# Kernel optimization log

Hardware: AMD Instinct MI355X
Metric: run time of the kernel (lower is better)

The kernel has to match this reference:

```python
import jax, jax.numpy as jnp
import numpy as np

N_NODES = 20000
N_EDGES = 320000
IN_DIM = 512
NUM_CLASSES = 10
DROP_P = 0.2


def _gcn_conv(x, src, dst, W, b, n):
    # PyG GCNConv: linear transform, add self-loops, symmetric deg^-1/2 norm,
    # scatter-add into destination nodes, then bias.
    h = x @ W                                   # [N, out]
    loops = jnp.arange(n)
    s = jnp.concatenate([src, loops])           # source (j)
    d = jnp.concatenate([dst, loops])           # destination (i)
    deg = jax.ops.segment_sum(jnp.ones_like(s, dtype=h.dtype), d, num_segments=n)
    dinv = jax.lax.rsqrt(deg)                   # deg >= 1 thanks to self-loops
    norm = dinv[s] * dinv[d]                    # [E+N]
    msg = h[s] * norm[:, None]                  # gather + per-edge scale
    out = jax.ops.segment_sum(msg, d, num_segments=n)  # scatter-add
    return out + b


def _dropout(x, key, p=DROP_P):
    keep = jax.random.bernoulli(key, 1.0 - p, x.shape)
    return jnp.where(keep, x / (1.0 - p), jnp.zeros((), x.dtype))


def setup_inputs() -> dict:
    key = jax.random.key(0)
    ks = jax.random.split(key, 6)
    x = jax.random.normal(ks[0], (N_NODES, IN_DIM), dtype=jnp.float32)
    edge_index = jax.random.randint(ks[1], (2, N_EDGES), 0, N_NODES, dtype=jnp.int64)
    h1, h2 = IN_DIM // 2, IN_DIM // 4
    W1 = jax.random.normal(ks[2], (IN_DIM, h1), dtype=jnp.float32) / np.sqrt(IN_DIM)
    W2 = jax.random.normal(ks[3], (h1, h2), dtype=jnp.float32) / np.sqrt(h1)
    W3 = jax.random.normal(ks[4], (h2, NUM_CLASSES), dtype=jnp.float32) / np.sqrt(h2)
    b1 = jnp.zeros((h1,), jnp.float32)
    b2 = jnp.zeros((h2,), jnp.float32)
    b3 = jnp.zeros((NUM_CLASSES,), jnp.float32)
    return {"x": x, "edge_index": edge_index, "W1": W1, "b1": b1,
            "W2": W2, "b2": b2, "W3": W3, "b3": b3}


def reference(x, edge_index, W1, b1, W2, b2, W3, b3):
    n = x.shape[0]
    src, dst = edge_index[0], edge_index[1]
    dk1, dk2 = jax.random.split(jax.random.key(1))
    h = _gcn_conv(x, src, dst, W1, b1, n)
    h = _dropout(jax.nn.relu(h), dk1)
    h = _gcn_conv(h, src, dst, W2, b2, n)
    h = _dropout(jax.nn.relu(h), dk2)
    h = _gcn_conv(h, src, dst, W3, b3, n)
    return jax.nn.log_softmax(h, axis=1)
```

## Files before the change

kernel.cpp:

```cpp
#include <hip/hip_runtime.h>
#include <hip/hip_bf16.h>
#include <math.h>

typedef __attribute__((ext_vector_type(8))) short short8;
typedef __attribute__((ext_vector_type(8))) unsigned short ushort8;
typedef __attribute__((ext_vector_type(4))) float f32x4;

__host__ __device__ inline void threefry2x32(unsigned k0, unsigned k1,
                                             unsigned x0, unsigned x1,
                                             unsigned* out0, unsigned* out1) {
  unsigned ks0 = k0, ks1 = k1, ks2 = k0 ^ k1 ^ 0x1BD11BDAu;
  x0 += ks0; x1 += ks1;
#define TF_ROUND(r) { x0 += x1; x1 = (x1 << (r)) | (x1 >> (32 - (r))); x1 ^= x0; }
  TF_ROUND(13) TF_ROUND(15) TF_ROUND(26) TF_ROUND(6)
  x0 += ks1; x1 += ks2 + 1u;
  TF_ROUND(17) TF_ROUND(29) TF_ROUND(16) TF_ROUND(24)
  x0 += ks2; x1 += ks0 + 2u;
  TF_ROUND(13) TF_ROUND(15) TF_ROUND(26) TF_ROUND(6)
  x0 += ks0; x1 += ks1 + 3u;
  TF_ROUND(17) TF_ROUND(29) TF_ROUND(16) TF_ROUND(24)
  x0 += ks1; x1 += ks2 + 4u;
  TF_ROUND(13) TF_ROUND(15) TF_ROUND(26) TF_ROUND(6)
  x0 += ks2; x1 += ks0 + 5u;
#undef TF_ROUND
  *out0 = x0; *out1 = x1;
}

__device__ inline float jax_uniform01(unsigned key0, unsigned key1, unsigned i) {
  unsigned o0, o1;
  threefry2x32(key0, key1, 0u, i, &o0, &o1);
  unsigned bits = o0 ^ o1;
  return __uint_as_float((bits >> 9) | 0x3f800000u) - 1.0f;
}

__device__ inline unsigned short f2bf(float f) {
  unsigned u = __float_as_uint(f);
  u += 0x7fffu + ((u >> 16) & 1u);
  return (unsigned short)(u >> 16);
}

__device__ inline float bf2f(unsigned short b) {
  return __uint_as_float(((unsigned)b) << 16);
}

__global__ void k_zero(int* p, int n) {
  int i = blockIdx.x * blockDim.x + threadIdx.x;
  if (i < n) p[i] = 0;
}

__global__ void k_deg(const int* __restrict__ ei, int E, int* __restrict__ deg) {
  int e = blockIdx.x * blockDim.x + threadIdx.x;
  if (e >= E) return;
  atomicAdd(&deg[ei[E + e]], 1);
}

__global__ __launch_bounds__(256) void k_bsum(const int* __restrict__ deg,
                                              int* __restrict__ bsum, int n) {
  int i = blockIdx.x * 256 + threadIdx.x;
  int v = (i < n) ? deg[i] : 0;
#pragma unroll
  for (int o = 32; o; o >>= 1) v += __shfl_down(v, o);
  __shared__ int ws[4];
  if ((threadIdx.x & 63) == 0) ws[threadIdx.x >> 6] = v;
  __syncthreads();
  if (threadIdx.x == 0) bsum[blockIdx.x] = ws[0] + ws[1] + ws[2] + ws[3];
}

__global__ void k_bscan(int* __restrict__ bsum, int nb) {
  __shared__ int s[128];
  int t = threadIdx.x;
  int v = (t < nb) ? bsum[t] : 0;
  s[t] = v;
  __syncthreads();
  for (int d = 1; d < 128; d <<= 1) {
    int u = (t >= d) ? s[t - d] : 0;
    __syncthreads();
    s[t] += u;
    __syncthreads();
  }
  if (t < nb) bsum[t] = (t == 0) ? 0 : s[t - 1];
}

__global__ __launch_bounds__(256) void k_scatter(const int* __restrict__ deg,
                                                 const int* __restrict__ bsum,
                                                 int* __restrict__ off, int* __restrict__ cur,
                                                 float* __restrict__ dinv, int n) {
  int i = blockIdx.x * 256 + threadIdx.x;
  int d = (i < n) ? deg[i] : 0;
  int lane = threadIdx.x & 63, w = threadIdx.x >> 6;
  int inc = d;
#pragma unroll
  for (int o = 1; o < 64; o <<= 1) {
    int u = __shfl_up(inc, o);
    if (lane >= o) inc += u;
  }
  __shared__ int wsum[4];
  if (lane == 63) wsum[w] = inc;
  __syncthreads();
  int wbase = 0;
  for (int k = 0; k < w; ++k) wbase += wsum[k];
  int excl = inc - d + wbase + bsum[blockIdx.x];
  if (i < n) {
    off[i] = excl;
    cur[i] = excl;
    dinv[i] = 1.0f / sqrtf((float)(d + 1));
    if (i == n - 1) off[n] = excl + d;
  }
}

__global__ void k_fill(const int* __restrict__ ei, int E,
                       int* __restrict__ cur, int* __restrict__ srcs) {
  int e = blockIdx.x * blockDim.x + threadIdx.x;
  if (e >= E) return;
  int s = ei[e];
  int d = ei[E + e];
  int pos = atomicAdd(&cur[d], 1);
  srcs[pos] = s;
}

__global__ void k_cvt_all(const float* __restrict__ W1, unsigned short* __restrict__ W1T,
                          const float* __restrict__ W2, unsigned short* __restrict__ W2T) {
  const int S1 = 512 * 256, S2 = 256 * 128;
  int idx = blockIdx.x * blockDim.x + threadIdx.x;
  if (idx < S1) {
    int k = idx / 256, n = idx % 256;
    W1T[(size_t)n * 512 + k] = f2bf(W1[idx]);
  } else if (idx < S1 + S2) {
    int i2 = idx - S1;
    int k = i2 / 128, n = i2 % 128;
    W2T[(size_t)n * 256 + k] = f2bf(W2[i2]);
  }
}

template <int NF, bool AF32, bool OBF>
__global__ __launch_bounds__(256) void k_gemm_mfma(const void* __restrict__ Ap,
                                                   const unsigned short* __restrict__ BT,
                                                   void* __restrict__ Cp,
                                                   int M, int N, int K) {
  constexpr int BN = 32 * NF;
  __shared__ unsigned short As[64][40];
  __shared__ unsigned short Bs[BN][40];
  const int tid = threadIdx.x;
  const int row0 = blockIdx.y * 64;
  const int col0 = blockIdx.x * BN;
  const int w = tid >> 6, lane = tid & 63;
  const int wm = w >> 1, wn = w & 1;
  const int lr = lane & 15, lk = lane >> 4;

  f32x4 acc[2][NF];
#pragma unroll
  for (int mi = 0; mi < 2; ++mi)
#pragma unroll
    for (int ni = 0; ni < NF; ++ni) acc[mi][ni] = (f32x4)0.0f;

  const int ar = tid >> 2;
  const int aseg = (tid & 3) * 8;

  for (int k0 = 0; k0 < K; k0 += 32) {
    {
      int grow = row0 + ar;
      ushort8 av = (ushort8)0;
      if (grow < M) {
        if (AF32) {
          const float* A = (const float*)Ap;
          const float* p = &A[(size_t)grow * K + k0 + aseg];
          float4 v0 = *(const float4*)p;
          float4 v1 = *(const float4*)(p + 4);
          av[0] = f2bf(v0.x); av[1] = f2bf(v0.y); av[2] = f2bf(v0.z); av[3] = f2bf(v0.w);
          av[4] = f2bf(v1.x); av[5] = f2bf(v1.y); av[6] = f2bf(v1.z); av[7] = f2bf(v1.w);
        } else {
          const unsigned short* A = (const unsigned short*)Ap;
          av = *(const ushort8*)&A[(size_t)grow * K + k0 + aseg];
        }
      }
      *(ushort8*)&As[ar][aseg] = av;
    }
#pragma unroll
    for (int p = 0; p < BN / 64; ++p) {
      int u = tid + p * 256;
      int br = u >> 2;
      int bseg = (u & 3) * 8;
      ushort8 bv = *(const ushort8*)&BT[(size_t)(col0 + br) * K + k0 + bseg];
      *(ushort8*)&Bs[br][bseg] = bv;
    }
    __syncthreads();

    short8 a[2], b[NF];
#pragma unroll
    for (int mi = 0; mi < 2; ++mi)
      a[mi] = *(const short8*)&As[wm * 32 + mi * 16 + lr][lk * 8];
#pragma unroll
    for (int ni = 0; ni < NF; ++ni)
      b[ni] = *(const short8*)&Bs[wn * (BN / 2) + ni * 16 + lr][lk * 8];
#pragma unroll
    for (int mi = 0; mi < 2; ++mi)
#pragma unroll
      for (int ni = 0; ni < NF; ++ni)
        acc[mi][ni] = __builtin_amdgcn_mfma_f32_16x16x32_bf16(a[mi], b[ni], acc[mi][ni], 0, 0, 0);
    __syncthreads();
  }

#pragma unroll
  for (int mi = 0; mi < 2; ++mi) {
    int rbase = row0 + wm * 32 + mi * 16 + lk * 4;
#pragma unroll
    for (int j = 0; j < 4; ++j) {
      int row = rbase + j;
      if (row < M) {
#pragma unroll
        for (int ni = 0; ni < NF; ++ni) {
          int col = col0 + wn * (BN / 2) + ni * 16 + lr;
          if (OBF) {
            ((unsigned short*)Cp)[(size_t)row * N + col] = f2bf(acc[mi][ni][j]);
          } else {
            ((float*)Cp)[(size_t)row * N + col] = acc[mi][ni][j];
          }
        }
      }
    }
  }
}

__global__ __launch_bounds__(256) void k_gemm(const float* __restrict__ A,
                                              const float* __restrict__ B,
                                              float* __restrict__ C,
                                              int M, int N, int K) {
  __shared__ float As[64][17];
  __shared__ float Bs[16][64];
  const int tid = threadIdx.x;
  const int tx = tid & 15, ty = tid >> 4;
  const int row0 = blockIdx.y * 64, col0 = blockIdx.x * 64;
  const int am = tid >> 2;
  const int aq = (tid & 3) * 4;
  const int bk = tid >> 4;
  const int bg = (tid & 15) * 4;
  const bool nvec = ((N & 3) == 0);
  float acc[4][4] = {{0.f}};

  for (int k0 = 0; k0 < K; k0 += 16) {
    {
      int row = row0 + am;
      if (row < M) {
        const float4 v = *reinterpret_cast<const float4*>(&A[(size_t)row * K + k0 + aq]);
        As[am][aq + 0] = v.x; As[am][aq + 1] = v.y;
        As[am][aq + 2] = v.z; As[am][aq + 3] = v.w;
      } else {
        As[am][aq + 0] = 0.f; As[am][aq + 1] = 0.f;
        As[am][aq + 2] = 0.f; As[am][aq + 3] = 0.f;
      }
    }
    {
      int krow = k0 + bk;
      if (nvec && (col0 + bg + 4 <= N)) {
        const float4 v = *reinterpret_cast<const float4*>(&B[(size_t)krow * N + col0 + bg]);
        Bs[bk][bg + 0] = v.x; Bs[bk][bg + 1] = v.y;
        Bs[bk][bg + 2] = v.z; Bs[bk][bg + 3] = v.w;
      } else {
        for (int j = 0; j < 4; ++j) {
          int col = col0 + bg + j;
          Bs[bk][bg + j] = (col < N) ? B[(size_t)krow * N + col] : 0.f;
        }
      }
    }
    __syncthreads();
#pragma unroll
    for (int kk = 0; kk < 16; ++kk) {
      float a0 = As[ty * 4 + 0][kk];
      float a1 = As[ty * 4 + 1][kk];
      float a2 = As[ty * 4 + 2][kk];
      float a3 = As[ty * 4 + 3][kk];
      float4 bv = *reinterpret_cast<const float4*>(&Bs[kk][tx * 4]);
      acc[0][0] += a0 * bv.x; acc[0][1] += a0 * bv.y; acc[0][2] += a0 * bv.z; acc[0][3] += a0 * bv.w;
      acc[1][0] += a1 * bv.x; acc[1][1] += a1 * bv.y; acc[1][2] += a1 * bv.z; acc[1][3] += a1 * bv.w;
      acc[2][0] += a2 * bv.x; acc[2][1] += a2 * bv.y; acc[2][2] += a2 * bv.z; acc[2][3] += a2 * bv.w;
      acc[3][0] += a3 * bv.x; acc[3][1] += a3 * bv.y; acc[3][2] += a3 * bv.z; acc[3][3] += a3 * bv.w;
    }
    __syncthreads();
  }

  for (int i = 0; i < 4; ++i) {
    int row = row0 + ty * 4 + i;
    if (row >= M) continue;
    for (int j = 0; j < 4; ++j) {
      int col = col0 + tx * 4 + j;
      if (col < N) C[(size_t)row * N + col] = acc[i][j];
    }
  }
}

template <int C, bool OBF>
__global__ __launch_bounds__(256) void k_agg_bf(const unsigned short* __restrict__ h,
                                                void* __restrict__ outv,
                                                const int* __restrict__ off,
                                                const int* __restrict__ srcs,
                                                const float* __restrict__ dinv,
                                                const float* __restrict__ bias,
                                                unsigned key0, unsigned key1, int n) {
  typedef __attribute__((ext_vector_type(C))) unsigned short ushortC;
  const int node = blockIdx.x * (blockDim.x >> 6) + (threadIdx.x >> 6);
  if (node >= n) return;
  const int lane = threadIdx.x & 63;
  const int F = 64 * C;
  const float dv = dinv[node];

  float acc[C];
  {
    ushortC r = *(const ushortC*)(h + (size_t)node * F + lane * C);
    float wv = dv * dv;
#pragma unroll
    for (int j = 0; j < C; ++j) acc[j] = bf2f(r[j]) * wv;
  }
  int e = off[node];
  const int e1 = off[node + 1];
  for (; e + 4 <= e1; e += 4) {
    int s0 = srcs[e + 0], s1 = srcs[e + 1], s2 = srcs[e + 2], s3 = srcs[e + 3];
    float w0 = dinv[s0] * dv, w1 = dinv[s1] * dv, w2 = dinv[s2] * dv, w3 = dinv[s3] * dv;
    ushortC r0 = *(const ushortC*)(h + (size_t)s0 * F + lane * C);
    ushortC r1 = *(const ushortC*)(h + (size_t)s1 * F + lane * C);
    ushortC r2 = *(const ushortC*)(h + (size_t)s2 * F + lane * C);
    ushortC r3 = *(const ushortC*)(h + (size_t)s3 * F + lane * C);
#pragma unroll
    for (int j = 0; j < C; ++j)
      acc[j] += bf2f(r0[j]) * w0 + bf2f(r1[j]) * w1 + bf2f(r2[j]) * w2 + bf2f(r3[j]) * w3;
  }
  for (; e < e1; ++e) {
    int s = srcs[e];
    float wv = dinv[s] * dv;
    ushortC r = *(const ushortC*)(h + (size_t)s * F + lane * C);
#pragma unroll
    for (int j = 0; j < C; ++j) acc[j] += bf2f(r[j]) * wv;
  }
#pragma unroll
  for (int j = 0; j < C; ++j) {
    float v = acc[j] + bias[lane * C + j];
    v = fmaxf(v, 0.0f);
    unsigned i = (unsigned)(node * F + lane * C + j);
    float u = jax_uniform01(key0, key1, i);
    v = (u < 0.8f) ? (v * 1.25f) : 0.0f;
    acc[j] = v;
  }
  if (OBF) {
    unsigned short* op = (unsigned short*)outv + (size_t)node * F + lane * C;
#pragma unroll
    for (int j = 0; j < C; ++j) op[j] = f2bf(acc[j]);
  } else {
    float* op = (float*)outv + (size_t)node * F + lane * C;
#pragma unroll
    for (int j = 0; j < C; ++j) op[j] = acc[j];
  }
}

__global__ __launch_bounds__(256) void k_agg3_lsm_v2(const float* __restrict__ h,
                                                     float* __restrict__ out,
                                                     const int* __restrict__ off,
                                                     const int* __restrict__ srcs,
                                                     const float* __restrict__ dinv,
                                                     const float* __restrict__ b,
                                                     int n) {
  const int node = blockIdx.x * 4 + (threadIdx.x >> 6);
  if (node >= n) return;
  const int lane = threadIdx.x & 63;
  const bool act = (lane < 10);
  const float dv = dinv[node];

  float acc = 0.0f;
  if (act) acc = h[(size_t)node * 10 + lane] * dv * dv;
  int e = off[node];
  const int e1 = off[node + 1];
  for (; e + 4 <= e1; e += 4) {
    int s0 = srcs[e + 0], s1 = srcs[e + 1], s2 = srcs[e + 2], s3 = srcs[e + 3];
    float w0 = dinv[s0] * dv, w1 = dinv[s1] * dv, w2 = dinv[s2] * dv, w3 = dinv[s3] * dv;
    if (act) {
      acc += h[(size_t)s0 * 10 + lane] * w0 + h[(size_t)s1 * 10 + lane] * w1 +
             h[(size_t)s2 * 10 + lane] * w2 + h[(size_t)s3 * 10 + lane] * w3;
    }
  }
  for (; e < e1; ++e) {
    int s = srcs[e];
    float w = dinv[s] * dv;
    if (act) acc += h[(size_t)s * 10 + lane] * w;
  }
  float v = act ? (acc + b[lane]) : -1e30f;
  float m = v;
#pragma unroll
  for (int o = 32; o; o >>= 1) m = fmaxf(m, __shfl_xor(m, o));
  float p = act ? expf(v - m) : 0.0f;
  float ssum = p;
#pragma unroll
  for (int o = 32; o; o >>= 1) ssum += __shfl_xor(ssum, o);
  float lse = m + logf(ssum);
  if (act) out[(size_t)node * 10 + lane] = v - lse;
}

extern "C" void kernel_launch(void* const* d_in, const int* in_sizes, int n_in,
                              void* d_out, int out_size, void* d_ws, size_t ws_size,
                              hipStream_t stream) {
  const float* x  = (const float*)d_in[0];
  const int*   ei = (const int*)d_in[1];
  const float* W1 = (const float*)d_in[2];
  const float* b1 = (const float*)d_in[3];
  const float* W2 = (const float*)d_in[4];
  const float* b2 = (const float*)d_in[5];
  const float* W3 = (const float*)d_in[6];
  const float* b3 = (const float*)d_in[7];
  float* out = (float*)d_out;

  const int N = 20000;
  const int E = in_sizes[1] / 2;
  const int D1 = 256, D2 = 128;
  const int NB = (N + 255) / 256;

  char* ws = (char*)d_ws;
  auto carve = [&](size_t bytes) -> char* {
    char* p = ws;
    ws += (bytes + 255) & ~(size_t)255;
    return p;
  };
  int*   deg  = (int*)carve((size_t)N * 4);
  int*   off  = (int*)carve((size_t)(N + 1) * 4);
  int*   cur  = (int*)carve((size_t)N * 4);
  float* dinv = (float*)carve((size_t)N * 4);
  int*   bsum = (int*)carve((size_t)128 * 4);
  int*   srcs = (int*)carve((size_t)E * 4);
  unsigned short* W1T = (unsigned short*)carve((size_t)D1 * 512 * 2);
  unsigned short* W2T = (unsigned short*)carve((size_t)D2 * D1 * 2);
  unsigned short* bufHb = (unsigned short*)carve((size_t)N * D1 * 2);
  unsigned short* bufA_bf = (unsigned short*)carve((size_t)N * D1 * 2);
  float* bufA2 = (float*)bufA_bf;
  float* bufH3 = (float*)carve((size_t)N * 10 * 4);

  unsigned dk1_0, dk1_1, dk2_0, dk2_1;
  threefry2x32(0u, 1u, 0u, 0u, &dk1_0, &dk1_1);
  threefry2x32(0u, 1u, 0u, 1u, &dk2_0, &dk2_1);

  k_zero<<<(N + 255) / 256, 256, 0, stream>>>(deg, N);
  k_deg<<<(E + 255) / 256, 256, 0, stream>>>(ei, E, deg);
  k_bsum<<<NB, 256, 0, stream>>>(deg, bsum, N);
  k_bscan<<<1, 128, 0, stream>>>(bsum, NB);
  k_scatter<<<NB, 256, 0, stream>>>(deg, bsum, off, cur, dinv, N);
  k_fill<<<(E + 255) / 256, 256, 0, stream>>>(ei, E, cur, srcs);
  k_cvt_all<<<(512 * 256 + 256 * 128 + 255) / 256, 256, 0, stream>>>(W1, W1T, W2, W2T);

  k_gemm_mfma<4, true, true><<<dim3(D1 / 128, (N + 63) / 64), 256, 0, stream>>>(x, W1T, bufHb, N, D1, 512);
  k_agg_bf<4, true><<<(N + 3) / 4, 256, 0, stream>>>(bufHb, bufA_bf, off, srcs, dinv, b1, dk1_0, dk1_1, N);

  k_gemm_mfma<4, false, true><<<dim3(D2 / 128, (N + 63) / 64), 256, 0, stream>>>(bufA_bf, W2T, bufHb, N, D2, D1);
  k_agg_bf<2, false><<<(N + 3) / 4, 256, 0, stream>>>(bufHb, bufA2, off, srcs, dinv, b2, dk2_0, dk2_1, N);

  k_gemm<<<dim3(1, (N + 63) / 64), 256, 0, stream>>>(bufA2, W3, bufH3, N, 10, D2);
  k_agg3_lsm_v2<<<(N + 3) / 4, 256, 0, stream>>>(bufH3, out, off, srcs, dinv, b3, N);
}
```

Baseline: 162.0 us.

## Precompute per-edge norm weights, merge setup kernels, deepen aggregation unroll

Stores a per-edge normalisation weight dinv[s]*dinv[d] in CSR order during the fill step, so the three aggregation kernels read a contiguous weight array instead of gathering dinv per edge. The degree zeroing and weight conversion are merged into one init kernel. The separate block scan is folded into the scatter kernel, which sums earlier block totals itself. The bf16 aggregation loop is unrolled to 8 edges to keep more gathers in flight. This adds an E-sized weight buffer and more registers per thread in exchange for fewer launches and fewer dependent random loads.

```diff
diff --git a/kernel.cpp b/kernel.cpp
--- a/kernel.cpp
+++ b/kernel.cpp
@@ -43,9 +43,25 @@
   return __uint_as_float(((unsigned)b) << 16);
 }
 
-__global__ void k_zero(int* p, int n) {
-  int i = blockIdx.x * blockDim.x + threadIdx.x;
-  if (i < n) p[i] = 0;
+__global__ __launch_bounds__(256) void k_init(int* __restrict__ deg, int n,
+                                              const float* __restrict__ W1,
+                                              unsigned short* __restrict__ W1T,
+                                              const float* __restrict__ W2,
+                                              unsigned short* __restrict__ W2T) {
+  const int S1 = 512 * 256, S2 = 256 * 128;
+  int idx = blockIdx.x * 256 + threadIdx.x;
+  if (idx < n) { deg[idx] = 0; return; }
+  idx -= n;
+  if (idx < S1) {
+    int k = idx / 256, c = idx % 256;
+    W1T[(size_t)c * 512 + k] = f2bf(W1[idx]);
+    return;
+  }
+  idx -= S1;
+  if (idx < S2) {
+    int k = idx / 128, c = idx % 128;
+    W2T[(size_t)c * 256 + k] = f2bf(W2[idx]);
+  }
 }
 
 __global__ void k_deg(const int* __restrict__ ei, int E, int* __restrict__ deg) {
@@ -66,28 +82,18 @@
   if (threadIdx.x == 0) bsum[blockIdx.x] = ws[0] + ws[1] + ws[2] + ws[3];
 }
 
-__global__ void k_bscan(int* __restrict__ bsum, int nb) {
-  __shared__ int s[128];
-  int t = threadIdx.x;
-  int v = (t < nb) ? bsum[t] : 0;
-  s[t] = v;
-  __syncthreads();
-  for (int d = 1; d < 128; d <<= 1) {
-    int u = (t >= d) ? s[t - d] : 0;
-    __syncthreads();
-    s[t] += u;
-    __syncthreads();
-  }
-  if (t < nb) bsum[t] = (t == 0) ? 0 : s[t - 1];
-}
-
-__global__ __launch_bounds__(256) void k_scatter(const int* __restrict__ deg,
-                                                 const int* __restrict__ bsum,
-                                                 int* __restrict__ off, int* __restrict__ cur,
-                                                 float* __restrict__ dinv, int n) {
+__global__ __launch_bounds__(256) void k_scatter2(const int* __restrict__ deg,
+                                                  const int* __restrict__ bsum,
+                                                  int* __restrict__ off, int* __restrict__ cur,
+                                                  float* __restrict__ dinv, int n) {
   int i = blockIdx.x * 256 + threadIdx.x;
+  int lane = threadIdx.x & 63, w = threadIdx.x >> 6;
+  int pb = 0;
+  for (int k = lane; k < blockIdx.x; k += 64) pb += bsum[k];
+#pragma unroll
+  for (int o = 32; o; o >>= 1) pb += __shfl_xor(pb, o);
+
   int d = (i < n) ? deg[i] : 0;
-  int lane = threadIdx.x & 63, w = threadIdx.x >> 6;
   int inc = d;
 #pragma unroll
   for (int o = 1; o < 64; o <<= 1) {
@@ -99,7 +105,7 @@
   __syncthreads();
   int wbase = 0;
   for (int k = 0; k < w; ++k) wbase += wsum[k];
-  int excl = inc - d + wbase + bsum[blockIdx.x];
+  int excl = inc - d + wbase + pb;
   if (i < n) {
     off[i] = excl;
     cur[i] = excl;
@@ -108,28 +114,16 @@
   }
 }
 
-__global__ void k_fill(const int* __restrict__ ei, int E,
-                       int* __restrict__ cur, int* __restrict__ srcs) {
+__global__ void k_fill_w(const int* __restrict__ ei, int E,
+                         int* __restrict__ cur, int* __restrict__ srcs,
+                         float* __restrict__ wgt, const float* __restrict__ dinv) {
   int e = blockIdx.x * blockDim.x + threadIdx.x;
   if (e >= E) return;
   int s = ei[e];
   int d = ei[E + e];
   int pos = atomicAdd(&cur[d], 1);
   srcs[pos] = s;
-}
-
-__global__ void k_cvt_all(const float* __restrict__ W1, unsigned short* __restrict__ W1T,
-                          const float* __restrict__ W2, unsigned short* __restrict__ W2T) {
-  const int S1 = 512 * 256, S2 = 256 * 128;
-  int idx = blockIdx.x * blockDim.x + threadIdx.x;
-  if (idx < S1) {
-    int k = idx / 256, n = idx % 256;
-    W1T[(size_t)n * 512 + k] = f2bf(W1[idx]);
-  } else if (idx < S1 + S2) {
-    int i2 = idx - S1;
-    int k = i2 / 128, n = i2 % 128;
-    W2T[(size_t)n * 256 + k] = f2bf(W2[i2]);
-  }
+  wgt[pos] = dinv[s] * dinv[d];
 }
 
 template <int NF, bool AF32, bool OBF>
@@ -293,6 +287,7 @@
                                                 void* __restrict__ outv,
                                                 const int* __restrict__ off,
                                                 const int* __restrict__ srcs,
+                                                const float* __restrict__ wgt,
                                                 const float* __restrict__ dinv,
                                                 const float* __restrict__ bias,
                                                 unsigned key0, unsigned key1, int n) {
@@ -312,20 +307,24 @@
   }
   int e = off[node];
   const int e1 = off[node + 1];
-  for (; e + 4 <= e1; e += 4) {
-    int s0 = srcs[e + 0], s1 = srcs[e + 1], s2 = srcs[e + 2], s3 = srcs[e + 3];
-    float w0 = dinv[s0] * dv, w1 = dinv[s1] * dv, w2 = dinv[s2] * dv, w3 = dinv[s3] * dv;
-    ushortC r0 = *(const ushortC*)(h + (size_t)s0 * F + lane * C);
-    ushortC r1 = *(const ushortC*)(h + (size_t)s1 * F + lane * C);
-    ushortC r2 = *(const ushortC*)(h + (size_t)s2 * F + lane * C);
-    ushortC r3 = *(const ushortC*)(h + (size_t)s3 * F + lane * C);
-#pragma unroll
-    for (int j = 0; j < C; ++j)
-      acc[j] += bf2f(r0[j]) * w0 + bf2f(r1[j]) * w1 + bf2f(r2[j]) * w2 + bf2f(r3[j]) * w3;
+  for (; e + 8 <= e1; e += 8) {
+    int s[8];
+    float wv[8];
+    ushortC r[8];
+#pragma unroll
+    for (int q = 0; q < 8; ++q) s[q] = srcs[e + q];
+#pragma unroll
+    for (int q = 0; q < 8; ++q) wv[q] = wgt[e + q];
+#pragma unroll
+    for (int q = 0; q < 8; ++q) r[q] = *(const ushortC*)(h + (size_t)s[q] * F + lane * C);
+#pragma unroll
+    for (int q = 0; q < 8; ++q)
+#pragma unroll
+      for (int j = 0; j < C; ++j) acc[j] += bf2f(r[q][j]) * wv[q];
   }
   for (; e < e1; ++e) {
     int s = srcs[e];
-    float wv = dinv[s] * dv;
+    float wv = wgt[e];
     ushortC r = *(const ushortC*)(h + (size_t)s * F + lane * C);
 #pragma unroll
     for (int j = 0; j < C; ++j) acc[j] += bf2f(r[j]) * wv;
@@ -354,6 +353,7 @@
                                                      float* __restrict__ out,
                                                      const int* __restrict__ off,
                                                      const int* __restrict__ srcs,
+                                                     const float* __restrict__ wgt,
                                                      const float* __restrict__ dinv,
                                                      const float* __restrict__ b,
                                                      int n) {
@@ -369,7 +369,7 @@
   const int e1 = off[node + 1];
   for (; e + 4 <= e1; e += 4) {
     int s0 = srcs[e + 0], s1 = srcs[e + 1], s2 = srcs[e + 2], s3 = srcs[e + 3];
-    float w0 = dinv[s0] * dv, w1 = dinv[s1] * dv, w2 = dinv[s2] * dv, w3 = dinv[s3] * dv;
+    float w0 = wgt[e + 0], w1 = wgt[e + 1], w2 = wgt[e + 2], w3 = wgt[e + 3];
     if (act) {
       acc += h[(size_t)s0 * 10 + lane] * w0 + h[(size_t)s1 * 10 + lane] * w1 +
              h[(size_t)s2 * 10 + lane] * w2 + h[(size_t)s3 * 10 + lane] * w3;
@@ -377,7 +377,7 @@
   }
   for (; e < e1; ++e) {
     int s = srcs[e];
-    float w = dinv[s] * dv;
+    float w = wgt[e];
     if (act) acc += h[(size_t)s * 10 + lane] * w;
   }
   float v = act ? (acc + b[lane]) : -1e30f;
@@ -422,6 +422,7 @@
   float* dinv = (float*)carve((size_t)N * 4);
   int*   bsum = (int*)carve((size_t)128 * 4);
   int*   srcs = (int*)carve((size_t)E * 4);
+  float* wgt  = (float*)carve((size_t)E * 4);
   unsigned short* W1T = (unsigned short*)carve((size_t)D1 * 512 * 2);
   unsigned short* W2T = (unsigned short*)carve((size_t)D2 * D1 * 2);
   unsigned short* bufHb = (unsigned short*)carve((size_t)N * D1 * 2);
@@ -433,20 +434,19 @@
   threefry2x32(0u, 1u, 0u, 0u, &dk1_0, &dk1_1);
   threefry2x32(0u, 1u, 0u, 1u, &dk2_0, &dk2_1);
 
-  k_zero<<<(N + 255) / 256, 256, 0, stream>>>(deg, N);
+  const int INIT_ITEMS = N + 512 * 256 + 256 * 128;
+  k_init<<<(INIT_ITEMS + 255) / 256, 256, 0, stream>>>(deg, N, W1, W1T, W2, W2T);
   k_deg<<<(E + 255) / 256, 256, 0, stream>>>(ei, E, deg);
   k_bsum<<<NB, 256, 0, stream>>>(deg, bsum, N);
-  k_bscan<<<1, 128, 0, stream>>>(bsum, NB);
-  k_scatter<<<NB, 256, 0, stream>>>(deg, bsum, off, cur, dinv, N);
-  k_fill<<<(E + 255) / 256, 256, 0, stream>>>(ei, E, cur, srcs);
-  k_cvt_all<<<(512 * 256 + 256 * 128 + 255) / 256, 256, 0, stream>>>(W1, W1T, W2, W2T);
+  k_scatter2<<<NB, 256, 0, stream>>>(deg, bsum, off, cur, dinv, N);
+  k_fill_w<<<(E + 255) / 256, 256, 0, stream>>>(ei, E, cur, srcs, wgt, dinv);
 
   k_gemm_mfma<4, true, true><<<dim3(D1 / 128, (N + 63) / 64), 256, 0, stream>>>(x, W1T, bufHb, N, D1, 512);
-  k_agg_bf<4, true><<<(N + 3) / 4, 256, 0, stream>>>(bufHb, bufA_bf, off, srcs, dinv, b1, dk1_0, dk1_1, N);
+  k_agg_bf<4, true><<<(N + 3) / 4, 256, 0, stream>>>(bufHb, bufA_bf, off, srcs, wgt, dinv, b1, dk1_0, dk1_1, N);
 
   k_gemm_mfma<4, false, true><<<dim3(D2 / 128, (N + 63) / 64), 256, 0, stream>>>(bufA_bf, W2T, bufHb, N, D2, D1);
-  k_agg_bf<2, false><<<(N + 3) / 4, 256, 0, stream>>>(bufHb, bufA2, off, srcs, dinv, b2, dk2_0, dk2_1, N);
+  k_agg_bf<2, false><<<(N + 3) / 4, 256, 0, stream>>>(bufHb, bufA2, off, srcs, wgt, dinv, b2, dk2_0, dk2_1, N);
 
   k_gemm<<<dim3(1, (N + 63) / 64), 256, 0, stream>>>(bufA2, W3, bufH3, N, 10, D2);
-  k_agg3_lsm_v2<<<(N + 3) / 4, 256, 0, stream>>>(bufH3, out, off, srcs, dinv, b3, N);
-}
+  k_agg3_lsm_v2<<<(N + 3) / 4, 256, 0, stream>>>(bufH3, out, off, srcs, wgt, dinv, b3, N);
+}
```

Result: no change. 160.2 us (-1.1%).
